# Kernel optimization log

Measured on AMD Instinct MI355X. Metric: run time of the kernel, lower is better.

## Reference

```python
import jax, jax.numpy as jnp
import numpy as np

B, T, C = 4, 4096, 1024
HEAD = 128


def setup_inputs() -> dict:
    key = jax.random.key(0)
    k0, k1, k2, k3 = jax.random.split(key, 4)
    x = jax.random.normal(k0, (B, T, C), dtype=jnp.float32)
    # bias-free linear weights, stored as (in, out) so y = x @ W
    Wk = jax.random.normal(k1, (C, HEAD), dtype=jnp.float32) * (C ** -0.5)
    Wq = jax.random.normal(k2, (C, HEAD), dtype=jnp.float32) * (C ** -0.5)
    Wv = jax.random.normal(k3, (C, HEAD), dtype=jnp.float32) * (C ** -0.5)
    return {"x": x, "Wk": Wk, "Wq": Wq, "Wv": Wv}


def reference(x, Wk, Wq, Wv):
    Bx, Tx, Cx = x.shape
    k = x @ Wk            # [B,T,H]
    q = x @ Wq            # [B,T,H]
    v = x @ Wv            # [B,T,H]
    # NOTE: original code scales by C**-0.5 where C = n_embd (input dim), not head_size
    scale = Cx ** -0.5
    wei = jnp.einsum("bqh,bkh->bqk", q, k) * scale        # [B,T,T]
    causal = jnp.arange(Tx)[:, None] >= jnp.arange(Tx)[None, :]
    wei = jnp.where(causal, wei, -jnp.inf)
    wei = jax.nn.softmax(wei, axis=-1)
    # dropout rate is 0.0 in the source -> identity
    return jnp.einsum("bqk,bkh->bqh", wei, v)             # [B,T,H]
```

## Files before the change

kernel.cpp:

```cpp
#include <hip/hip_runtime.h>


typedef __bf16 bf16;
typedef bf16 bf16x8 __attribute__((ext_vector_type(8)));
typedef bf16 bf16x4 __attribute__((ext_vector_type(4)));
typedef float f32x4 __attribute__((ext_vector_type(4)));

#define L2E 1.4426950408889634f
#define TSEQ 4096
#define CDIM 1024
#define HDIM 128
#define MROWS 16384

#define GLDS(g, l)                                              \
  __builtin_amdgcn_global_load_lds(                             \
      (__attribute__((address_space(1))) void*)(g),             \
      (__attribute__((address_space(3))) void*)(l), 16, 0, 0)

static __device__ inline unsigned pkbf(float a, float b) {
  union { bf16 h; unsigned short u; } ua, ub;
  ua.h = (bf16)a; ub.h = (bf16)b;
  return ((unsigned)ub.u << 16) | (unsigned)ua.u;
}

__global__ __launch_bounds__(256) void wt_prep(const float* __restrict__ Wq,
                                               const float* __restrict__ Wk,
                                               const float* __restrict__ Wv,
                                               bf16* __restrict__ WT) {
  const int mode = blockIdx.y;
  const float* W = (mode == 0) ? Wq : (mode == 1) ? Wk : Wv;
  const int idx = blockIdx.x * 256 + threadIdx.x;
  const int n = idx >> 10;
  const int k = idx & 1023;
  WT[(size_t)mode * 131072 + idx] = (bf16)W[(size_t)k * HDIM + n];
}

__global__ __launch_bounds__(256) void qkv_gemm(const float* __restrict__ x,
                                                const bf16* __restrict__ WT,
                                                bf16* __restrict__ qb,
                                                bf16* __restrict__ kb,
                                                bf16* __restrict__ vT) {
  __shared__ __attribute__((aligned(16))) bf16 a_tile[128 * 32];
  __shared__ __attribute__((aligned(16))) bf16 b_tile[128 * 32];
  const int tid = threadIdx.x;
  const int wid = tid >> 6;
  const int lane = tid & 63;
  const int lr = lane & 15;
  const int lg = lane >> 4;
  const int wr = wid >> 1;
  const int wc = wid & 1;
  const int mode = blockIdx.y;
  const int m0 = blockIdx.x * 128;
  const bf16* wt = WT + (size_t)mode * 131072;

  int rowA[2], col8[2];
#pragma unroll
  for (int g = 0; g < 2; ++g) {
    const int idx8 = g * 256 + tid;
    rowA[g] = idx8 >> 2;
    col8[g] = (idx8 & 3) * 8;
  }

  f32x4 acc[4][4] = {};

  float4 fA[2][2];
  bf16x8 fB[2];
#pragma unroll
  for (int g = 0; g < 2; ++g) {
    const float* src = x + (size_t)(m0 + rowA[g]) * CDIM + col8[g];
    fA[g][0] = *(const float4*)src;
    fA[g][1] = *(const float4*)(src + 4);
    fB[g] = *(const bf16x8*)(wt + (size_t)rowA[g] * CDIM + col8[g]);
  }

#pragma unroll 1
  for (int kt = 0; kt < 32; ++kt) {
    __syncthreads();
#pragma unroll
    for (int g = 0; g < 2; ++g) {
      bf16x8 av;
      av[0] = (bf16)fA[g][0].x; av[1] = (bf16)fA[g][0].y;
      av[2] = (bf16)fA[g][0].z; av[3] = (bf16)fA[g][0].w;
      av[4] = (bf16)fA[g][1].x; av[5] = (bf16)fA[g][1].y;
      av[6] = (bf16)fA[g][1].z; av[7] = (bf16)fA[g][1].w;
      *(bf16x8*)&a_tile[rowA[g] * 32 + col8[g]] = av;
      *(bf16x8*)&b_tile[rowA[g] * 32 + col8[g]] = fB[g];
    }
    __syncthreads();
    if (kt + 1 < 32) {
#pragma unroll
      for (int g = 0; g < 2; ++g) {
        const float* src = x + (size_t)(m0 + rowA[g]) * CDIM + (kt + 1) * 32 + col8[g];
        fA[g][0] = *(const float4*)src;
        fA[g][1] = *(const float4*)(src + 4);
        fB[g] = *(const bf16x8*)(wt + (size_t)rowA[g] * CDIM + (kt + 1) * 32 + col8[g]);
      }
    }
    bf16x8 af[4], bfr[4];
#pragma unroll
    for (int r = 0; r < 4; ++r)
      af[r] = *(const bf16x8*)&a_tile[(wr * 64 + r * 16 + lr) * 32 + lg * 8];
#pragma unroll
    for (int c = 0; c < 4; ++c)
      bfr[c] = *(const bf16x8*)&b_tile[(wc * 64 + c * 16 + lr) * 32 + lg * 8];
#pragma unroll
    for (int r = 0; r < 4; ++r)
#pragma unroll
      for (int c = 0; c < 4; ++c)
        acc[r][c] = __builtin_amdgcn_mfma_f32_16x16x32_bf16(af[r], bfr[c], acc[r][c], 0, 0, 0);
  }

  if (mode < 2) {
    bf16* dst = (mode == 0) ? qb : kb;
    const float sc = (mode == 0) ? 0.03125f : 1.0f;
#pragma unroll
    for (int r = 0; r < 4; ++r)
#pragma unroll
      for (int c = 0; c < 4; ++c)
#pragma unroll
        for (int j = 0; j < 4; ++j) {
          const int row = m0 + wr * 64 + r * 16 + lg * 4 + j;
          const int col = wc * 64 + c * 16 + lr;
          dst[(size_t)row * HDIM + col] = (bf16)(acc[r][c][j] * sc);
        }
  } else {
#pragma unroll
    for (int r = 0; r < 4; ++r)
#pragma unroll
      for (int c = 0; c < 4; ++c) {
        const int row0 = m0 + wr * 64 + r * 16 + lg * 4;
        const int col = wc * 64 + c * 16 + lr;
        bf16x4 pv;
        pv[0] = (bf16)acc[r][c][0]; pv[1] = (bf16)acc[r][c][1];
        pv[2] = (bf16)acc[r][c][2]; pv[3] = (bf16)acc[r][c][3];
        *(bf16x4*)(vT + (size_t)(row0 >> 6) * 8192 + col * 64 + (row0 & 63)) = pv;
      }
  }
}

__global__ __launch_bounds__(512, 4) void attn_part(const bf16* __restrict__ qg,
                                                    const bf16* __restrict__ kb,
                                                    const bf16* __restrict__ vT,
                                                    bf16* __restrict__ po,
                                                    float* __restrict__ pm,
                                                    float* __restrict__ pl,
                                                    int cshift, int maxc) {
  __shared__ __attribute__((aligned(16))) char kv_lds[2][32768];
  __shared__ __attribute__((aligned(16))) bf16 p_lds[8][16][64];
  const int tid = threadIdx.x;
  const int wid = tid >> 6;
  const int lane = tid & 63;
  const int lr = lane & 15;
  const int lg = lane >> 4;
  const int b = blockIdx.z;
  const int c = blockIdx.y;
  const int qbase = blockIdx.x * 128;
  const int kv0 = c << cshift;
  if (kv0 >= qbase + 128) return;
  const int kvend = min(kv0 + (1 << cshift), qbase + 128);
  const int nt = (kvend - kv0) >> 6;
  const int qr0 = qbase + wid * 16;
  const int grp = blockIdx.x * 8 + wid;
  const size_t qrow = (size_t)b * TSEQ + qr0;

  const int wbase = wid * 2048;
  int ksrc[2], vsrc[2];
#pragma unroll
  for (int i = 0; i < 2; ++i) {
    const int o = wbase + i * 1024 + lane * 16;
    const int rk = o >> 8;
    ksrc[i] = rk * 256 + ((o & 255) ^ ((rk & 7) << 4));
    const int rv = o >> 7;
    vsrc[i] = rv * 128 + ((o & 127) ^ ((rv & 7) << 4));
  }
  const char* kgb = (const char*)kb + (size_t)b * TSEQ * 256;
  const char* vgb = (const char*)vT + (size_t)b * TSEQ * 256;

  const int msk = (lr & 7) << 4;
  const int m30 = (lr & 3) << 4;
  const int m6 = (lr & 4) << 4;
  const int lgx = (lg * 16) ^ m30;
  const int kreadA = lr * 256 + lgx + m6;
  const int kreadB = lr * 256 + lgx + (64 ^ m6);
  const int vreadA = 16384 + lr * 128 + lgx + m6;
  const int vreadB = 16384 + lr * 128 + lgx + (64 ^ m6);

  bf16x8 qf[4];
#pragma unroll
  for (int d = 0; d < 4; ++d)
    qf[d] = *(const bf16x8*)(qg + (qrow + lr) * HDIM + d * 32 + lg * 8);

  f32x4 o_[8] = {};
  float m_ = -1e30f, l_ = 0.0f;

  {
    const char* ks = kgb + (size_t)kv0 * 256;
    const char* vs = vgb + (size_t)kv0 * 256;
#pragma unroll
    for (int i = 0; i < 2; ++i) {
      GLDS(ks + ksrc[i], &kv_lds[0][wbase + i * 1024]);
      GLDS(vs + vsrc[i], &kv_lds[0][16384 + wbase + i * 1024]);
    }
  }
  __syncthreads();

  int cur = 0;
  for (int t = 0; t < nt; ++t) {
    const int kvt = kv0 + (t << 6);
    if (t + 1 < nt) {
      const char* ks = kgb + (size_t)(kvt + 64) * 256;
      const char* vs = vgb + (size_t)(kvt + 64) * 256;
#pragma unroll
      for (int i = 0; i < 2; ++i) {
        GLDS(ks + ksrc[i], &kv_lds[cur ^ 1][wbase + i * 1024]);
        GLDS(vs + vsrc[i], &kv_lds[cur ^ 1][16384 + wbase + i * 1024]);
      }
    }
    if (kvt < qr0 + 16) {
      const char* kbuf = kv_lds[cur];
      f32x4 s[4] = {};
      __builtin_amdgcn_s_setprio(1);
#pragma unroll
      for (int nf = 0; nf < 4; ++nf) {
        const char* kb0 = kbuf + nf * 4096;
        bf16x8 kf;
        kf = *(const bf16x8*)(kb0 + kreadA);
        s[nf] = __builtin_amdgcn_mfma_f32_16x16x32_bf16(kf, qf[0], s[nf], 0, 0, 0);
        kf = *(const bf16x8*)(kb0 + kreadB);
        s[nf] = __builtin_amdgcn_mfma_f32_16x16x32_bf16(kf, qf[1], s[nf], 0, 0, 0);
        kf = *(const bf16x8*)(kb0 + kreadA + 128);
        s[nf] = __builtin_amdgcn_mfma_f32_16x16x32_bf16(kf, qf[2], s[nf], 0, 0, 0);
        kf = *(const bf16x8*)(kb0 + kreadB + 128);
        s[nf] = __builtin_amdgcn_mfma_f32_16x16x32_bf16(kf, qf[3], s[nf], 0, 0, 0);
      }
      __builtin_amdgcn_s_setprio(0);
      if (kvt + 63 >= qr0) {
        const int q = qr0 + lr;
#pragma unroll
        for (int nf = 0; nf < 4; ++nf)
#pragma unroll
          for (int j = 0; j < 4; ++j)
            if (kvt + nf * 16 + lg * 4 + j > q) s[nf][j] = -1e30f;
      }
      float rloc = fmaxf(fmaxf(s[0][0], s[0][1]), fmaxf(s[0][2], s[0][3]));
#pragma unroll
      for (int nf = 1; nf < 4; ++nf)
        rloc = fmaxf(rloc, fmaxf(fmaxf(s[nf][0], s[nf][1]), fmaxf(s[nf][2], s[nf][3])));
      if (!__all(rloc <= m_ + 8.0f)) {
        float rmax = fmaxf(rloc, __shfl_xor(rloc, 16));
        rmax = fmaxf(rmax, __shfl_xor(rmax, 32));
        const float mn = fmaxf(m_, rmax);
        const float al = exp2f((m_ - mn) * L2E);
        m_ = mn;
        l_ *= al;
#pragma unroll
        for (int o = 0; o < 8; ++o)
#pragma unroll
          for (int j = 0; j < 4; ++j) o_[o][j] *= al;
      }
      float rsum = 0.0f;
#pragma unroll
      for (int nf = 0; nf < 4; ++nf)
#pragma unroll
        for (int j = 0; j < 4; ++j) {
          s[nf][j] = exp2f((s[nf][j] - m_) * L2E);
          rsum += s[nf][j];
        }
      l_ += rsum;
      {
        char* pw = (char*)p_lds + wid * 2048 + lr * 128;
#pragma unroll
        for (int nf = 0; nf < 4; ++nf) {
          uint2 w2;
          w2.x = pkbf(s[nf][0], s[nf][1]); w2.y = pkbf(s[nf][2], s[nf][3]);
          *(uint2*)(pw + (((nf * 32) + lg * 8) ^ msk)) = w2;
        }
      }
      asm volatile("s_waitcnt lgkmcnt(0)" ::: "memory");
      __builtin_amdgcn_sched_barrier(0);
      const char* pr = (const char*)p_lds + wid * 2048 + lr * 128;
      bf16x8 pf0 = *(const bf16x8*)(pr + lgx + m6);
      bf16x8 pf1 = *(const bf16x8*)(pr + lgx + (64 ^ m6));
      __builtin_amdgcn_s_setprio(1);
#pragma unroll
      for (int o = 0; o < 8; ++o) {
        bf16x8 vf;
        vf = *(const bf16x8*)(kbuf + vreadA + o * 2048);
        o_[o] = __builtin_amdgcn_mfma_f32_16x16x32_bf16(vf, pf0, o_[o], 0, 0, 0);
        vf = *(const bf16x8*)(kbuf + vreadB + o * 2048);
        o_[o] = __builtin_amdgcn_mfma_f32_16x16x32_bf16(vf, pf1, o_[o], 0, 0, 0);
      }
      __builtin_amdgcn_s_setprio(0);
    }
    __syncthreads();
    cur ^= 1;
  }

  l_ += __shfl_xor(l_, 16);
  l_ += __shfl_xor(l_, 32);

  const size_t slot = (size_t)(b * 256 + grp) * maxc + c;
  bf16* pob = po + slot * (16 * HDIM);
#pragma unroll
  for (int o = 0; o < 8; ++o) {
    bf16x4 pv;
    pv[0] = (bf16)o_[o][0]; pv[1] = (bf16)o_[o][1];
    pv[2] = (bf16)o_[o][2]; pv[3] = (bf16)o_[o][3];
    *(bf16x4*)(pob + lr * HDIM + o * 16 + lg * 4) = pv;
  }
  if (lg == 0) {
    pm[slot * 16 + lr] = m_;
    pl[slot * 16 + lr] = l_;
  }
}

__global__ __launch_bounds__(256) void attn_merge(const bf16* __restrict__ po,
                                                  const float* __restrict__ pm,
                                                  const float* __restrict__ pl,
                                                  float* __restrict__ out,
                                                  int cshift, int maxc) {
  const int bg = blockIdx.x;
  const int g = bg & 255;
  const int nch = ((g << 4) >> cshift) + 1;
  const int row = threadIdx.x >> 4;
  const int d8 = (threadIdx.x & 15) * 8;
  const size_t slot0 = (size_t)bg * maxc;

  float M = -1e30f;
  for (int c = 0; c < nch; ++c) M = fmaxf(M, pm[(slot0 + c) * 16 + row]);
  float L = 0.0f;
  float acc[8] = {};
  for (int c = 0; c < nch; ++c) {
    const float w = exp2f((pm[(slot0 + c) * 16 + row] - M) * L2E);
    L += w * pl[(slot0 + c) * 16 + row];
    const bf16x8 v = *(const bf16x8*)(po + (slot0 + c) * (16 * HDIM) + row * HDIM + d8);
#pragma unroll
    for (int i = 0; i < 8; ++i) acc[i] += w * (float)v[i];
  }
  const float inv = 1.0f / L;
  f32x4 r0, r1;
#pragma unroll
  for (int i = 0; i < 4; ++i) { r0[i] = acc[i] * inv; r1[i] = acc[i + 4] * inv; }
  float* dst = out + (size_t)bg * (16 * HDIM) + row * HDIM + d8;
  *(f32x4*)dst = r0;
  *(f32x4*)(dst + 4) = r1;
}

extern "C" void kernel_launch(void* const* d_in, const int* in_sizes, int n_in,
                              void* d_out, int out_size, void* d_ws, size_t ws_size,
                              hipStream_t stream) {
  const float* x  = (const float*)d_in[0];
  const float* Wk = (const float*)d_in[1];
  const float* Wq = (const float*)d_in[2];
  const float* Wv = (const float*)d_in[3];
  float* out = (float*)d_out;

  char* ws = (char*)d_ws;
  bf16* qb = (bf16*)(ws);
  bf16* kb = (bf16*)(ws + 4194304);
  bf16* vT = (bf16*)(ws + 8388608);
  bf16* WT = (bf16*)(ws + 12582912);
  const size_t pbase = 13369344;

  int cshift, maxc;
  if (ws_size >= pbase + 8ull * 1024 * 4224) { cshift = 9;  maxc = 8; }
  else if (ws_size >= pbase + 4ull * 1024 * 4224) { cshift = 10; maxc = 4; }
  else { cshift = 12; maxc = 1; }
  bf16* po = (bf16*)(ws + pbase);
  float* pm = (float*)(ws + pbase + (size_t)maxc * 1024 * 16 * 128 * 2);
  float* pl = pm + (size_t)maxc * 1024 * 16;

  wt_prep<<<dim3(512, 3), 256, 0, stream>>>(Wq, Wk, Wv, WT);
  qkv_gemm<<<dim3(128, 3), 256, 0, stream>>>(x, WT, qb, kb, vT);
  attn_part<<<dim3(32, maxc, 4), 512, 0, stream>>>(qb, kb, vT, po, pm, pl, cshift, maxc);
  attn_merge<<<1024, 256, 0, stream>>>(po, pm, pl, out, cshift, maxc);
}
```

Measured before the change: 98.05 us.

## Load V fragments directly from global into registers instead of staging through LDS

```diff
diff --git a/kernel.cpp b/kernel.cpp
--- a/kernel.cpp
+++ b/kernel.cpp
@@ -145,7 +145,7 @@
                                                     float* __restrict__ pm,
                                                     float* __restrict__ pl,
                                                     int cshift, int maxc) {
-  __shared__ __attribute__((aligned(16))) char kv_lds[2][32768];
+  __shared__ __attribute__((aligned(16))) char kv_lds[2][16384];
   __shared__ __attribute__((aligned(16))) bf16 p_lds[8][16][64];
   const int tid = threadIdx.x;
   const int wid = tid >> 6;
@@ -164,17 +164,15 @@
   const size_t qrow = (size_t)b * TSEQ + qr0;
 
   const int wbase = wid * 2048;
-  int ksrc[2], vsrc[2];
+  int ksrc[2];
 #pragma unroll
   for (int i = 0; i < 2; ++i) {
     const int o = wbase + i * 1024 + lane * 16;
     const int rk = o >> 8;
     ksrc[i] = rk * 256 + ((o & 255) ^ ((rk & 7) << 4));
-    const int rv = o >> 7;
-    vsrc[i] = rv * 128 + ((o & 127) ^ ((rv & 7) << 4));
   }
   const char* kgb = (const char*)kb + (size_t)b * TSEQ * 256;
-  const char* vgb = (const char*)vT + (size_t)b * TSEQ * 256;
+  const bf16* vtb = vT + (size_t)b * 64 * 8192;
 
   const int msk = (lr & 7) << 4;
   const int m30 = (lr & 3) << 4;
@@ -182,8 +180,6 @@
   const int lgx = (lg * 16) ^ m30;
   const int kreadA = lr * 256 + lgx + m6;
   const int kreadB = lr * 256 + lgx + (64 ^ m6);
-  const int vreadA = 16384 + lr * 128 + lgx + m6;
-  const int vreadB = 16384 + lr * 128 + lgx + (64 ^ m6);
 
   bf16x8 qf[4];
 #pragma unroll
@@ -195,12 +191,8 @@
 
   {
     const char* ks = kgb + (size_t)kv0 * 256;
-    const char* vs = vgb + (size_t)kv0 * 256;
-#pragma unroll
-    for (int i = 0; i < 2; ++i) {
-      GLDS(ks + ksrc[i], &kv_lds[0][wbase + i * 1024]);
-      GLDS(vs + vsrc[i], &kv_lds[0][16384 + wbase + i * 1024]);
-    }
+#pragma unroll
+    for (int i = 0; i < 2; ++i) GLDS(ks + ksrc[i], &kv_lds[0][wbase + i * 1024]);
   }
   __syncthreads();
 
@@ -209,15 +201,18 @@
     const int kvt = kv0 + (t << 6);
     if (t + 1 < nt) {
       const char* ks = kgb + (size_t)(kvt + 64) * 256;
-      const char* vs = vgb + (size_t)(kvt + 64) * 256;
-#pragma unroll
-      for (int i = 0; i < 2; ++i) {
-        GLDS(ks + ksrc[i], &kv_lds[cur ^ 1][wbase + i * 1024]);
-        GLDS(vs + vsrc[i], &kv_lds[cur ^ 1][16384 + wbase + i * 1024]);
-      }
+#pragma unroll
+      for (int i = 0; i < 2; ++i) GLDS(ks + ksrc[i], &kv_lds[cur ^ 1][wbase + i * 1024]);
     }
     if (kvt < qr0 + 16) {
       const char* kbuf = kv_lds[cur];
+      const bf16* vt = vtb + (size_t)(kvt >> 6) * 8192 + lr * 64 + lg * 8;
+      bf16x8 vf[8][2];
+#pragma unroll
+      for (int o = 0; o < 8; ++o) {
+        vf[o][0] = *(const bf16x8*)(vt + o * 1024);
+        vf[o][1] = *(const bf16x8*)(vt + o * 1024 + 32);
+      }
       f32x4 s[4] = {};
       __builtin_amdgcn_s_setprio(1);
 #pragma unroll
@@ -284,11 +279,8 @@
       __builtin_amdgcn_s_setprio(1);
 #pragma unroll
       for (int o = 0; o < 8; ++o) {
-        bf16x8 vf;
-        vf = *(const bf16x8*)(kbuf + vreadA + o * 2048);
-        o_[o] = __builtin_amdgcn_mfma_f32_16x16x32_bf16(vf, pf0, o_[o], 0, 0, 0);
-        vf = *(const bf16x8*)(kbuf + vreadB + o * 2048);
-        o_[o] = __builtin_amdgcn_mfma_f32_16x16x32_bf16(vf, pf1, o_[o], 0, 0, 0);
+        o_[o] = __builtin_amdgcn_mfma_f32_16x16x32_bf16(vf[o][0], pf0, o_[o], 0, 0, 0);
+        o_[o] = __builtin_amdgcn_mfma_f32_16x16x32_bf16(vf[o][1], pf1, o_[o], 0, 0, 0);
       }
       __builtin_amdgcn_s_setprio(0);
     }
```

Result: slower. 245.3 us (+150.2%).

## Load projection weights via global_load_lds and remap attention blocks across XCDs

Applied to the files above, without the earlier changes.

```diff
diff --git a/kernel.cpp b/kernel.cpp
--- a/kernel.cpp
+++ b/kernel.cpp
@@ -60,17 +60,22 @@
     rowA[g] = idx8 >> 2;
     col8[g] = (idx8 & 3) * 8;
   }
+  int bsrc[2], bdst[2];
+#pragma unroll
+  for (int i = 0; i < 2; ++i) {
+    const int db = i * 4096 + tid * 16;
+    bdst[i] = db;
+    bsrc[i] = (db >> 6) * 2048 + (db & 63);
+  }
 
   f32x4 acc[4][4] = {};
 
   float4 fA[2][2];
-  bf16x8 fB[2];
 #pragma unroll
   for (int g = 0; g < 2; ++g) {
     const float* src = x + (size_t)(m0 + rowA[g]) * CDIM + col8[g];
     fA[g][0] = *(const float4*)src;
     fA[g][1] = *(const float4*)(src + 4);
-    fB[g] = *(const bf16x8*)(wt + (size_t)rowA[g] * CDIM + col8[g]);
   }
 
 #pragma unroll 1
@@ -84,8 +89,10 @@
       av[4] = (bf16)fA[g][1].x; av[5] = (bf16)fA[g][1].y;
       av[6] = (bf16)fA[g][1].z; av[7] = (bf16)fA[g][1].w;
       *(bf16x8*)&a_tile[rowA[g] * 32 + col8[g]] = av;
-      *(bf16x8*)&b_tile[rowA[g] * 32 + col8[g]] = fB[g];
-    }
+    }
+#pragma unroll
+    for (int i = 0; i < 2; ++i)
+      GLDS((const char*)wt + bsrc[i] + kt * 64, (char*)b_tile + bdst[i]);
     __syncthreads();
     if (kt + 1 < 32) {
 #pragma unroll
@@ -93,7 +100,6 @@
         const float* src = x + (size_t)(m0 + rowA[g]) * CDIM + (kt + 1) * 32 + col8[g];
         fA[g][0] = *(const float4*)src;
         fA[g][1] = *(const float4*)(src + 4);
-        fB[g] = *(const bf16x8*)(wt + (size_t)rowA[g] * CDIM + (kt + 1) * 32 + col8[g]);
       }
     }
     bf16x8 af[4], bfr[4];
@@ -152,15 +158,25 @@
   const int lane = tid & 63;
   const int lr = lane & 15;
   const int lg = lane >> 4;
-  const int b = blockIdx.z;
-  const int c = blockIdx.y;
-  const int qbase = blockIdx.x * 128;
+
+  int bx = blockIdx.x, c = blockIdx.y, b = blockIdx.z;
+  if (maxc == 8) {
+    const int p = blockIdx.x + 32 * (blockIdx.y + 8 * blockIdx.z);
+    const int xcd = p & 7;
+    const int s = p >> 3;
+    const int combo = s >> 5;
+    bx = s & 31;
+    b = combo;
+    c = (combo < 2) ? xcd : 7 - xcd;
+  }
+
+  const int qbase = bx * 128;
   const int kv0 = c << cshift;
   if (kv0 >= qbase + 128) return;
   const int kvend = min(kv0 + (1 << cshift), qbase + 128);
   const int nt = (kvend - kv0) >> 6;
   const int qr0 = qbase + wid * 16;
-  const int grp = blockIdx.x * 8 + wid;
+  const int grp = bx * 8 + wid;
   const size_t qrow = (size_t)b * TSEQ + qr0;
 
   const int wbase = wid * 2048;
```

Result: no change. 97.29 us (-0.8%).
